# Kernel optimization log

Hardware: AMD Instinct MI355X
Metric: run time of the kernel (lower is better)

## Reference

```python
import jax, jax.numpy as jnp
import numpy as np

HIDDEN = 128
EDGE = 64
EPS = 1e-5

def setup_inputs() -> dict:
    key = jax.random.key(0)
    ks = jax.random.split(key, 12)
    B, N, D = 8, 256, HIDDEN
    h = jax.random.normal(ks[0], (B, N, D), dtype=jnp.float32)
    edge_feats = jax.random.normal(ks[1], (B, N, N, 3), dtype=jnp.float32)
    adj_mask = jax.random.bernoulli(ks[2], 0.5, (B, N, N))
    s = lambda fan_in: 1.0 / np.sqrt(fan_in)
    W1 = jax.random.uniform(ks[3], (D + 3, EDGE), minval=-s(D + 3), maxval=s(D + 3))
    b1 = jnp.zeros((EDGE,), jnp.float32)
    W2 = jax.random.uniform(ks[4], (EDGE, D), minval=-s(EDGE), maxval=s(EDGE))
    b2 = jnp.zeros((D,), jnp.float32)
    U1 = jax.random.uniform(ks[5], (3 * D, D), minval=-s(3 * D), maxval=s(3 * D))
    b3 = jnp.zeros((D,), jnp.float32)
    U2 = jax.random.uniform(ks[6], (D, D), minval=-s(D), maxval=s(D))
    b4 = jnp.zeros((D,), jnp.float32)
    gamma = jnp.ones((D,), jnp.float32)
    beta = jnp.zeros((D,), jnp.float32)
    return {"h": h, "edge_feats": edge_feats, "adj_mask": adj_mask,
            "W1": W1, "b1": b1, "W2": W2, "b2": b2,
            "U1": U1, "b3": b3, "U2": U2, "b4": b4,
            "gamma": gamma, "beta": beta}

def reference(h, edge_feats, adj_mask, W1, b1, W2, b2, U1, b3, U2, b4, gamma, beta):
    B, N, D = h.shape
    # NOTE: torch does h.unsqueeze(2).expand(B,N,N,D): h_j[b,i,j,:] = h[b,i,:]
    h_j = jnp.broadcast_to(h[:, :, None, :], (B, N, N, D))
    gate_in = jnp.concatenate([h_j, edge_feats], axis=-1)          # (B,N,N,D+3)
    gates = jax.nn.sigmoid(jax.nn.relu(gate_in @ W1 + b1) @ W2 + b2)  # (B,N,N,D)
    mask_f = adj_mask.astype(h.dtype)[..., None]                    # (B,N,N,1)
    messages = gates * h_j * mask_f
    neighbor_count = jnp.clip(jnp.sum(mask_f, axis=2), 1.0)         # (B,N,1)
    agg_mean = jnp.sum(messages, axis=2) / neighbor_count           # (B,N,D)
    msgs_max = jnp.where(adj_mask[..., None], messages, -jnp.inf)
    agg_max = jnp.max(msgs_max, axis=2)
    agg_max = jnp.where(jnp.isinf(agg_max), 0.0, agg_max)
    upd_in = jnp.concatenate([h, agg_mean, agg_max], axis=-1)       # (B,N,3D)
    upd = jax.nn.relu(upd_in @ U1 + b3) @ U2 + b4
    x = h + upd
    mu = jnp.mean(x, axis=-1, keepdims=True)
    var = jnp.var(x, axis=-1, keepdims=True)
    return (x - mu) * jax.lax.rsqrt(var + EPS) * gamma + beta
```

## Files before the change

kernel.cpp:

```cpp
#include <hip/hip_runtime.h>
#include <hip/hip_bf16.h>
#include <math.h>

#define NN 256
#define DD 128
#define EE 64
#define TPAD 72
#define APAD 392
#define RPAD 136

typedef __attribute__((ext_vector_type(8))) short short8;
typedef __attribute__((ext_vector_type(4))) float f32x4;

static __device__ __forceinline__ unsigned short f2bf(float f) {
    __hip_bfloat16 b = __float2bfloat16(f);
    return *reinterpret_cast<unsigned short*>(&b);
}

static __device__ __forceinline__ short8 ldb(const float* __restrict__ B, int kbase, int d) {
    unsigned short tmp[8];
    #pragma unroll
    for (int j = 0; j < 8; ++j) tmp[j] = f2bf(B[(kbase + j) * DD + d]);
    return *(const short8*)tmp;
}

__global__ __launch_bounds__(256, 3)
void ecgc_gate(const float* __restrict__ h_g,
               const float* __restrict__ ef_g,
               const int*   __restrict__ mask_g,
               const float* __restrict__ W1_g,
               const float* __restrict__ b1_g,
               const float* __restrict__ W2_g,
               const float* __restrict__ b2_g,
               float*       __restrict__ ws)
{
    const int bi   = blockIdx.x;
    const int t    = threadIdx.x;
    const int lane = t & 63;
    const int w    = t >> 6;
    const int m16  = lane & 15;
    const int quad = lane >> 4;

    __shared__ __align__(16) unsigned short shT[NN * TPAD];
    __shared__ __align__(16) float sh_ef[NN * 4];
    __shared__ float sh_h[DD], sh_base[EE], sh_w1e[3 * EE];
    __shared__ int   sh_jlist[NN], sh_wcnt[4], sh_cnt;

    if (t < DD) sh_h[t] = h_g[bi * DD + t];
    {
        const float* efr = ef_g + (size_t)bi * NN * 3;
        sh_ef[t * 4 + 0] = efr[t * 3 + 0];
        sh_ef[t * 4 + 1] = efr[t * 3 + 1];
        sh_ef[t * 4 + 2] = efr[t * 3 + 2];
        sh_ef[t * 4 + 3] = 0.f;
    }
    const int mk = (mask_g[bi * NN + t] != 0) ? 1 : 0;
    const unsigned long long bal = __ballot(mk);
    if (lane == 0) sh_wcnt[w] = __popcll(bal);
    const int pre = __popcll(bal & ((1ull << lane) - 1ull));
    __syncthreads();

    {
        int wbase = 0;
        for (int ww = 0; ww < w; ++ww) wbase += sh_wcnt[ww];
        if (mk) sh_jlist[wbase + pre] = t;
        if (t == 0) sh_cnt = sh_wcnt[0] + sh_wcnt[1] + sh_wcnt[2] + sh_wcnt[3];
    }

    if (t < EE) {
        float acc = b1_g[t];
        #pragma unroll 4
        for (int d = 0; d < DD; ++d)
            acc = fmaf(sh_h[d], W1_g[d * EE + t], acc);
        sh_base[t] = acc;
    } else {
        const int u = t - EE;
        sh_w1e[u] = W1_g[(DD + (u >> 6)) * EE + (u & 63)];
    }

    const int dstripe = w * 32;
    short8 bfrag[2][2];
    float  nb2[2];
    #pragma unroll
    for (int dt = 0; dt < 2; ++dt) {
        const int d = dstripe + 16 * dt + m16;
        nb2[dt] = b2_g[d];
        #pragma unroll
        for (int kh = 0; kh < 2; ++kh)
            bfrag[dt][kh] = ldb(W2_g, kh * 32 + quad * 8, d);
    }
    __syncthreads();

    const int cnt = sh_cnt;
    const int njt = (cnt + 15) >> 4;

    {
        const int cj = t & 63, eg = w;
        for (int c = 0; c < 4; ++c) {
            const int js = c * 64 + cj;
            float e0 = 0.f, e1 = 0.f, e2 = 0.f;
            const int ok = (js < cnt);
            if (ok) {
                const float4 efv = *(const float4*)&sh_ef[sh_jlist[js] * 4];
                e0 = efv.x; e1 = efv.y; e2 = efv.z;
            }
            unsigned short pk[16];
            #pragma unroll
            for (int v = 0; v < 16; ++v) {
                const int e = eg * 16 + v;
                float tv = 0.f;
                if (ok)
                    tv = fmaxf(fmaf(e0, sh_w1e[e],
                               fmaf(e1, sh_w1e[64 + e],
                               fmaf(e2, sh_w1e[128 + e], sh_base[e]))), 0.f);
                pk[v] = f2bf(tv);
            }
            *(short8*)&shT[js * TPAD + eg * 16]     = *(const short8*)&pk[0];
            *(short8*)&shT[js * TPAD + eg * 16 + 8] = *(const short8*)&pk[8];
        }
    }
    __syncthreads();

    float sumv[2] = {0.f, 0.f};
    float mxv[2]  = {-__builtin_inff(), -__builtin_inff()};
    float mnv[2]  = { __builtin_inff(),  __builtin_inff()};

    for (int jt = 0; jt < njt; ++jt) {
        const short8 a0 = *(const short8*)&shT[(jt * 16 + m16) * TPAD + quad * 8];
        const short8 a1 = *(const short8*)&shT[(jt * 16 + m16) * TPAD + 32 + quad * 8];
        const int jbase = jt * 16 + quad * 4;
        #pragma unroll
        for (int dt = 0; dt < 2; ++dt) {
            f32x4 acc = {0.f, 0.f, 0.f, 0.f};
            acc = __builtin_amdgcn_mfma_f32_16x16x32_bf16(a0, bfrag[dt][0], acc, 0, 0, 0);
            acc = __builtin_amdgcn_mfma_f32_16x16x32_bf16(a1, bfrag[dt][1], acc, 0, 0, 0);
            #pragma unroll
            for (int r = 0; r < 4; ++r) {
                const float g = __fdividef(1.f, 1.f + __expf(-(acc[r] + nb2[dt])));
                if (jbase + r < cnt) {
                    sumv[dt] += g;
                    mxv[dt]  = fmaxf(mxv[dt], g);
                    mnv[dt]  = fminf(mnv[dt], g);
                }
            }
        }
    }

    #pragma unroll
    for (int dt = 0; dt < 2; ++dt) {
        float s = sumv[dt], M = mxv[dt], mn = mnv[dt];
        s += __shfl_xor(s, 16, 64);  s += __shfl_xor(s, 32, 64);
        M  = fmaxf(M,  __shfl_xor(M, 16, 64));  M  = fmaxf(M,  __shfl_xor(M, 32, 64));
        mn = fminf(mn, __shfl_xor(mn, 16, 64)); mn = fminf(mn, __shfl_xor(mn, 32, 64));
        if (quad == 0) {
            const int d  = dstripe + 16 * dt + m16;
            const float hd = sh_h[d];
            float mean = 0.f, amax = 0.f;
            if (cnt > 0) {
                mean = hd * s * __fdividef(1.f, (float)cnt);
                amax = (hd >= 0.f) ? hd * M : hd * mn;
            }
            ws[bi * 256 + d]       = mean;
            ws[bi * 256 + 128 + d] = amax;
        }
    }
}

__global__ __launch_bounds__(256, 2)
void ecgc_upd(const float* __restrict__ h_g,
              const float* __restrict__ ws,
              const float* __restrict__ U1_g,
              const float* __restrict__ b3_g,
              const float* __restrict__ U2_g,
              const float* __restrict__ b4_g,
              const float* __restrict__ gam_g,
              const float* __restrict__ bet_g,
              float*       __restrict__ out_g)
{
    const int bi0  = blockIdx.x * 32;
    const int t    = threadIdx.x;
    const int lane = t & 63;
    const int w    = t >> 6;
    const int m16  = lane & 15;
    const int quad = lane >> 4;

    __shared__ __align__(16) unsigned short shA[32 * APAD];
    __shared__ __align__(16) unsigned short rbuf[32 * RPAD];
    __shared__ float sh_s[4 * 32], sh_s2[4 * 32], sh_mu[32], sh_rs[32];

    {
        const int row = t >> 3, q = t & 7;
        const float* srcs[3] = { h_g + (size_t)(bi0 + row) * DD + q * 16,
                                 ws  + (size_t)(bi0 + row) * 256 + q * 16,
                                 ws  + (size_t)(bi0 + row) * 256 + 128 + q * 16 };
        #pragma unroll
        for (int seg = 0; seg < 3; ++seg) {
            const float4* sp = (const float4*)srcs[seg];
            unsigned short tmp[16];
            #pragma unroll
            for (int vv = 0; vv < 4; ++vv) {
                const float4 v = sp[vv];
                tmp[vv * 4 + 0] = f2bf(v.x); tmp[vv * 4 + 1] = f2bf(v.y);
                tmp[vv * 4 + 2] = f2bf(v.z); tmp[vv * 4 + 3] = f2bf(v.w);
            }
            *(short8*)&shA[row * APAD + seg * DD + q * 16]     = *(const short8*)&tmp[0];
            *(short8*)&shA[row * APAD + seg * DD + q * 16 + 8] = *(const short8*)&tmp[8];
        }
    }
    __syncthreads();

    const int dstripe = w * 32;

    f32x4 acc[2][2];
    #pragma unroll
    for (int mt = 0; mt < 2; ++mt)
        #pragma unroll
        for (int dt = 0; dt < 2; ++dt) acc[mt][dt] = (f32x4){0.f, 0.f, 0.f, 0.f};

    for (int kk = 0; kk < 12; ++kk) {
        const short8 a0 = *(const short8*)&shA[m16 * APAD + kk * 32 + quad * 8];
        const short8 a1 = *(const short8*)&shA[(16 + m16) * APAD + kk * 32 + quad * 8];
        #pragma unroll
        for (int dt = 0; dt < 2; ++dt) {
            const short8 b = ldb(U1_g, kk * 32 + quad * 8, dstripe + dt * 16 + m16);
            acc[0][dt] = __builtin_amdgcn_mfma_f32_16x16x32_bf16(a0, b, acc[0][dt], 0, 0, 0);
            acc[1][dt] = __builtin_amdgcn_mfma_f32_16x16x32_bf16(a1, b, acc[1][dt], 0, 0, 0);
        }
    }

    #pragma unroll
    for (int mt = 0; mt < 2; ++mt)
        #pragma unroll
        for (int dt = 0; dt < 2; ++dt) {
            const int d = dstripe + dt * 16 + m16;
            const float bb = b3_g[d];
            #pragma unroll
            for (int r = 0; r < 4; ++r) {
                const int ro = mt * 16 + quad * 4 + r;
                rbuf[ro * RPAD + d] = f2bf(fmaxf(acc[mt][dt][r] + bb, 0.f));
            }
        }
    __syncthreads();

    f32x4 acc2[2][2];
    #pragma unroll
    for (int mt = 0; mt < 2; ++mt)
        #pragma unroll
        for (int dt = 0; dt < 2; ++dt) acc2[mt][dt] = (f32x4){0.f, 0.f, 0.f, 0.f};

    for (int kk = 0; kk < 4; ++kk) {
        const short8 a0 = *(const short8*)&rbuf[m16 * RPAD + kk * 32 + quad * 8];
        const short8 a1 = *(const short8*)&rbuf[(16 + m16) * RPAD + kk * 32 + quad * 8];
        #pragma unroll
        for (int dt = 0; dt < 2; ++dt) {
            const short8 b = ldb(U2_g, kk * 32 + quad * 8, dstripe + dt * 16 + m16);
            acc2[0][dt] = __builtin_amdgcn_mfma_f32_16x16x32_bf16(a0, b, acc2[0][dt], 0, 0, 0);
            acc2[1][dt] = __builtin_amdgcn_mfma_f32_16x16x32_bf16(a1, b, acc2[1][dt], 0, 0, 0);
        }
    }

    float xv[2][2][4];
    #pragma unroll
    for (int mt = 0; mt < 2; ++mt)
        #pragma unroll
        for (int dt = 0; dt < 2; ++dt) {
            const int d = dstripe + dt * 16 + m16;
            const float bb = b4_g[d];
            #pragma unroll
            for (int r = 0; r < 4; ++r) {
                const int ro = mt * 16 + quad * 4 + r;
                xv[mt][dt][r] = h_g[(size_t)(bi0 + ro) * DD + d] + acc2[mt][dt][r] + bb;
            }
        }

    #pragma unroll
    for (int mt = 0; mt < 2; ++mt)
        #pragma unroll
        for (int r = 0; r < 4; ++r) {
            float s  = xv[mt][0][r] + xv[mt][1][r];
            float s2 = xv[mt][0][r] * xv[mt][0][r] + xv[mt][1][r] * xv[mt][1][r];
            #pragma unroll
            for (int off = 1; off < 16; off <<= 1) {
                s  += __shfl_xor(s,  off, 64);
                s2 += __shfl_xor(s2, off, 64);
            }
            if (m16 == 0) {
                const int ro = mt * 16 + quad * 4 + r;
                sh_s[w * 32 + ro]  = s;
                sh_s2[w * 32 + ro] = s2;
            }
        }
    __syncthreads();
    if (t < 32) {
        const float S  = sh_s[t]  + sh_s[32 + t]  + sh_s[64 + t]  + sh_s[96 + t];
        const float S2 = sh_s2[t] + sh_s2[32 + t] + sh_s2[64 + t] + sh_s2[96 + t];
        const float mu  = S * (1.f / 128.f);
        const float var = S2 * (1.f / 128.f) - mu * mu;
        sh_mu[t] = mu;
        sh_rs[t] = rsqrtf(var + 1e-5f);
    }
    __syncthreads();

    #pragma unroll
    for (int mt = 0; mt < 2; ++mt)
        #pragma unroll
        for (int dt = 0; dt < 2; ++dt) {
            const int d = dstripe + dt * 16 + m16;
            const float ga = gam_g[d], be = bet_g[d];
            #pragma unroll
            for (int r = 0; r < 4; ++r) {
                const int ro = mt * 16 + quad * 4 + r;
                out_g[(size_t)(bi0 + ro) * DD + d] =
                    (xv[mt][dt][r] - sh_mu[ro]) * sh_rs[ro] * ga + be;
            }
        }
}

extern "C" void kernel_launch(void* const* d_in, const int* in_sizes, int n_in,
                              void* d_out, int out_size, void* d_ws, size_t ws_size,
                              hipStream_t stream) {
    float* ws = (float*)d_ws;
    ecgc_gate<<<8 * NN, 256, 0, stream>>>(
        (const float*)d_in[0],
        (const float*)d_in[1],
        (const int*)d_in[2],
        (const float*)d_in[3],
        (const float*)d_in[4],
        (const float*)d_in[5],
        (const float*)d_in[6],
        ws);
    ecgc_upd<<<(8 * NN) / 32, 256, 0, stream>>>(
        (const float*)d_in[0],
        ws,
        (const float*)d_in[7],
        (const float*)d_in[8],
        (const float*)d_in[9],
        (const float*)d_in[10],
        (const float*)d_in[11],
        (const float*)d_in[12],
        (float*)d_out);
}
```

Measured before the change: 140.1 us.

## Chunk gate tile to shrink LDS, parallelize base GEMV, halve upd block rows

Result: faster. 125.5 us (-10.4%).

```diff
diff --git a/kernel.cpp b/kernel.cpp
--- a/kernel.cpp
+++ b/kernel.cpp
@@ -24,7 +24,7 @@
     return *(const short8*)tmp;
 }
 
-__global__ __launch_bounds__(256, 3)
+__global__ __launch_bounds__(256, 6)
 void ecgc_gate(const float* __restrict__ h_g,
                const float* __restrict__ ef_g,
                const int*   __restrict__ mask_g,
@@ -41,12 +41,16 @@
     const int m16  = lane & 15;
     const int quad = lane >> 4;
 
-    __shared__ __align__(16) unsigned short shT[NN * TPAD];
+    __shared__ __align__(16) unsigned short shT[64 * TPAD];
     __shared__ __align__(16) float sh_ef[NN * 4];
-    __shared__ float sh_h[DD], sh_base[EE], sh_w1e[3 * EE];
+    __shared__ __align__(16) float sh_base[EE];
+    __shared__ __align__(16) float sh_w1e[3 * EE];
+    __shared__ float sh_h[DD];
+    __shared__ float sh_basep[4 * EE];
     __shared__ int   sh_jlist[NN], sh_wcnt[4], sh_cnt;
 
     if (t < DD) sh_h[t] = h_g[bi * DD + t];
+    if (t < 192) sh_w1e[t] = W1_g[(DD + (t >> 6)) * EE + (t & 63)];
     {
         const float* efr = ef_g + (size_t)bi * NN * 3;
         sh_ef[t * 4 + 0] = efr[t * 3 + 0];
@@ -58,6 +62,18 @@
     const unsigned long long bal = __ballot(mk);
     if (lane == 0) sh_wcnt[w] = __popcll(bal);
     const int pre = __popcll(bal & ((1ull << lane) - 1ull));
+
+    const int dstripe = w * 32;
+    short8 bfrag[2][2];
+    float  nb2[2];
+    #pragma unroll
+    for (int dt = 0; dt < 2; ++dt) {
+        const int d = dstripe + 16 * dt + m16;
+        nb2[dt] = b2_g[d];
+        #pragma unroll
+        for (int kh = 0; kh < 2; ++kh)
+            bfrag[dt][kh] = ldb(W2_g, kh * 32 + quad * 8, d);
+    }
     __syncthreads();
 
     {
@@ -66,84 +82,86 @@
         if (mk) sh_jlist[wbase + pre] = t;
         if (t == 0) sh_cnt = sh_wcnt[0] + sh_wcnt[1] + sh_wcnt[2] + sh_wcnt[3];
     }
-
-    if (t < EE) {
-        float acc = b1_g[t];
+    {
+        const int e = t & 63, dgrp = t >> 6;
+        float acc = 0.f;
         #pragma unroll 4
-        for (int d = 0; d < DD; ++d)
-            acc = fmaf(sh_h[d], W1_g[d * EE + t], acc);
-        sh_base[t] = acc;
-    } else {
-        const int u = t - EE;
-        sh_w1e[u] = W1_g[(DD + (u >> 6)) * EE + (u & 63)];
-    }
-
-    const int dstripe = w * 32;
-    short8 bfrag[2][2];
-    float  nb2[2];
-    #pragma unroll
-    for (int dt = 0; dt < 2; ++dt) {
-        const int d = dstripe + 16 * dt + m16;
-        nb2[dt] = b2_g[d];
-        #pragma unroll
-        for (int kh = 0; kh < 2; ++kh)
-            bfrag[dt][kh] = ldb(W2_g, kh * 32 + quad * 8, d);
-    }
+        for (int d = dgrp * 32; d < dgrp * 32 + 32; ++d)
+            acc = fmaf(sh_h[d], W1_g[d * EE + e], acc);
+        sh_basep[dgrp * EE + e] = acc;
+    }
+    __syncthreads();
+    if (t < EE)
+        sh_base[t] = b1_g[t] + sh_basep[t] + sh_basep[EE + t] +
+                     sh_basep[2 * EE + t] + sh_basep[3 * EE + t];
     __syncthreads();
 
     const int cnt = sh_cnt;
-    const int njt = (cnt + 15) >> 4;
-
-    {
-        const int cj = t & 63, eg = w;
-        for (int c = 0; c < 4; ++c) {
-            const int js = c * 64 + cj;
-            float e0 = 0.f, e1 = 0.f, e2 = 0.f;
-            const int ok = (js < cnt);
+    const int nch = (cnt + 63) >> 6;
+
+    float sumv[2] = {0.f, 0.f};
+    float mxv[2]  = {-__builtin_inff(), -__builtin_inff()};
+    float mnv[2]  = { __builtin_inff(),  __builtin_inff()};
+
+    for (int ch = 0; ch < nch; ++ch) {
+        {
+            const int row = t >> 2, e0 = (t & 3) * 16;
+            const int js  = ch * 64 + row;
+            const int ok  = (js < cnt);
+            float e0f = 0.f, e1f = 0.f, e2f = 0.f;
             if (ok) {
                 const float4 efv = *(const float4*)&sh_ef[sh_jlist[js] * 4];
-                e0 = efv.x; e1 = efv.y; e2 = efv.z;
+                e0f = efv.x; e1f = efv.y; e2f = efv.z;
             }
             unsigned short pk[16];
             #pragma unroll
-            for (int v = 0; v < 16; ++v) {
-                const int e = eg * 16 + v;
-                float tv = 0.f;
-                if (ok)
-                    tv = fmaxf(fmaf(e0, sh_w1e[e],
-                               fmaf(e1, sh_w1e[64 + e],
-                               fmaf(e2, sh_w1e[128 + e], sh_base[e]))), 0.f);
-                pk[v] = f2bf(tv);
-            }
-            *(short8*)&shT[js * TPAD + eg * 16]     = *(const short8*)&pk[0];
-            *(short8*)&shT[js * TPAD + eg * 16 + 8] = *(const short8*)&pk[8];
-        }
-    }
-    __syncthreads();
-
-    float sumv[2] = {0.f, 0.f};
-    float mxv[2]  = {-__builtin_inff(), -__builtin_inff()};
-    float mnv[2]  = { __builtin_inff(),  __builtin_inff()};
-
-    for (int jt = 0; jt < njt; ++jt) {
-        const short8 a0 = *(const short8*)&shT[(jt * 16 + m16) * TPAD + quad * 8];
-        const short8 a1 = *(const short8*)&shT[(jt * 16 + m16) * TPAD + 32 + quad * 8];
-        const int jbase = jt * 16 + quad * 4;
-        #pragma unroll
-        for (int dt = 0; dt < 2; ++dt) {
-            f32x4 acc = {0.f, 0.f, 0.f, 0.f};
-            acc = __builtin_amdgcn_mfma_f32_16x16x32_bf16(a0, bfrag[dt][0], acc, 0, 0, 0);
-            acc = __builtin_amdgcn_mfma_f32_16x16x32_bf16(a1, bfrag[dt][1], acc, 0, 0, 0);
-            #pragma unroll
-            for (int r = 0; r < 4; ++r) {
-                const float g = __fdividef(1.f, 1.f + __expf(-(acc[r] + nb2[dt])));
-                if (jbase + r < cnt) {
-                    sumv[dt] += g;
-                    mxv[dt]  = fmaxf(mxv[dt], g);
-                    mnv[dt]  = fminf(mnv[dt], g);
+            for (int vb = 0; vb < 4; ++vb) {
+                const float4 bs = *(const float4*)&sh_base[e0 + vb * 4];
+                const float4 w0 = *(const float4*)&sh_w1e[e0 + vb * 4];
+                const float4 w1 = *(const float4*)&sh_w1e[64 + e0 + vb * 4];
+                const float4 w2 = *(const float4*)&sh_w1e[128 + e0 + vb * 4];
+                const float bsx[4] = {bs.x, bs.y, bs.z, bs.w};
+                const float w0x[4] = {w0.x, w0.y, w0.z, w0.w};
+                const float w1x[4] = {w1.x, w1.y, w1.z, w1.w};
+                const float w2x[4] = {w2.x, w2.y, w2.z, w2.w};
+                #pragma unroll
+                for (int v = 0; v < 4; ++v) {
+                    float tv = 0.f;
+                    if (ok)
+                        tv = fmaxf(fmaf(e0f, w0x[v],
+                                   fmaf(e1f, w1x[v],
+                                   fmaf(e2f, w2x[v], bsx[v]))), 0.f);
+                    pk[vb * 4 + v] = f2bf(tv);
                 }
             }
-        }
+            *(short8*)&shT[row * TPAD + e0]     = *(const short8*)&pk[0];
+            *(short8*)&shT[row * TPAD + e0 + 8] = *(const short8*)&pk[8];
+        }
+        __syncthreads();
+
+        const int rem = min(64, cnt - ch * 64);
+        const int jtn = (rem + 15) >> 4;
+        for (int jt = 0; jt < jtn; ++jt) {
+            const short8 a0 = *(const short8*)&shT[(jt * 16 + m16) * TPAD + quad * 8];
+            const short8 a1 = *(const short8*)&shT[(jt * 16 + m16) * TPAD + 32 + quad * 8];
+            const int jbase = ch * 64 + jt * 16 + quad * 4;
+            #pragma unroll
+            for (int dt = 0; dt < 2; ++dt) {
+                f32x4 acc = {0.f, 0.f, 0.f, 0.f};
+                acc = __builtin_amdgcn_mfma_f32_16x16x32_bf16(a0, bfrag[dt][0], acc, 0, 0, 0);
+                acc = __builtin_amdgcn_mfma_f32_16x16x32_bf16(a1, bfrag[dt][1], acc, 0, 0, 0);
+                #pragma unroll
+                for (int r = 0; r < 4; ++r) {
+                    const float g = __fdividef(1.f, 1.f + __expf(-(acc[r] + nb2[dt])));
+                    if (jbase + r < cnt) {
+                        sumv[dt] += g;
+                        mxv[dt]  = fmaxf(mxv[dt], g);
+                        mnv[dt]  = fminf(mnv[dt], g);
+                    }
+                }
+            }
+        }
+        __syncthreads();
     }
 
     #pragma unroll
@@ -177,123 +195,102 @@
               const float* __restrict__ bet_g,
               float*       __restrict__ out_g)
 {
-    const int bi0  = blockIdx.x * 32;
+    const int bi0  = blockIdx.x * 16;
     const int t    = threadIdx.x;
     const int lane = t & 63;
     const int w    = t >> 6;
     const int m16  = lane & 15;
     const int quad = lane >> 4;
 
-    __shared__ __align__(16) unsigned short shA[32 * APAD];
-    __shared__ __align__(16) unsigned short rbuf[32 * RPAD];
-    __shared__ float sh_s[4 * 32], sh_s2[4 * 32], sh_mu[32], sh_rs[32];
+    __shared__ __align__(16) unsigned short shA[16 * APAD];
+    __shared__ __align__(16) unsigned short rbuf[16 * RPAD];
+    __shared__ float sh_s[4 * 16], sh_s2[4 * 16], sh_mu[16], sh_rs[16];
 
     {
-        const int row = t >> 3, q = t & 7;
-        const float* srcs[3] = { h_g + (size_t)(bi0 + row) * DD + q * 16,
-                                 ws  + (size_t)(bi0 + row) * 256 + q * 16,
-                                 ws  + (size_t)(bi0 + row) * 256 + 128 + q * 16 };
-        #pragma unroll
-        for (int seg = 0; seg < 3; ++seg) {
-            const float4* sp = (const float4*)srcs[seg];
-            unsigned short tmp[16];
-            #pragma unroll
-            for (int vv = 0; vv < 4; ++vv) {
-                const float4 v = sp[vv];
-                tmp[vv * 4 + 0] = f2bf(v.x); tmp[vv * 4 + 1] = f2bf(v.y);
-                tmp[vv * 4 + 2] = f2bf(v.z); tmp[vv * 4 + 3] = f2bf(v.w);
-            }
-            *(short8*)&shA[row * APAD + seg * DD + q * 16]     = *(const short8*)&tmp[0];
-            *(short8*)&shA[row * APAD + seg * DD + q * 16 + 8] = *(const short8*)&tmp[8];
-        }
+        const int row = t >> 4, q = t & 15;
+        const float* hrow = h_g + (size_t)(bi0 + row) * DD;
+        const float* wrow = ws  + (size_t)(bi0 + row) * 256;
+        unsigned short tmp[24];
+        #pragma unroll
+        for (int c = 0; c < 24; ++c) {
+            const int col = q * 24 + c;
+            float v;
+            if (col < 128)      v = hrow[col];
+            else if (col < 256) v = wrow[col - 128];
+            else                v = wrow[col - 256 + 128];
+            tmp[c] = f2bf(v);
+        }
+        #pragma unroll
+        for (int s8 = 0; s8 < 3; ++s8)
+            *(short8*)&shA[row * APAD + q * 24 + s8 * 8] = *(const short8*)&tmp[s8 * 8];
     }
     __syncthreads();
 
     const int dstripe = w * 32;
 
-    f32x4 acc[2][2];
-    #pragma unroll
-    for (int mt = 0; mt < 2; ++mt)
-        #pragma unroll
-        for (int dt = 0; dt < 2; ++dt) acc[mt][dt] = (f32x4){0.f, 0.f, 0.f, 0.f};
-
+    f32x4 acc[2] = {{0.f, 0.f, 0.f, 0.f}, {0.f, 0.f, 0.f, 0.f}};
     for (int kk = 0; kk < 12; ++kk) {
         const short8 a0 = *(const short8*)&shA[m16 * APAD + kk * 32 + quad * 8];
-        const short8 a1 = *(const short8*)&shA[(16 + m16) * APAD + kk * 32 + quad * 8];
         #pragma unroll
         for (int dt = 0; dt < 2; ++dt) {
             const short8 b = ldb(U1_g, kk * 32 + quad * 8, dstripe + dt * 16 + m16);
-            acc[0][dt] = __builtin_amdgcn_mfma_f32_16x16x32_bf16(a0, b, acc[0][dt], 0, 0, 0);
-            acc[1][dt] = __builtin_amdgcn_mfma_f32_16x16x32_bf16(a1, b, acc[1][dt], 0, 0, 0);
-        }
-    }
-
-    #pragma unroll
-    for (int mt = 0; mt < 2; ++mt)
-        #pragma unroll
-        for (int dt = 0; dt < 2; ++dt) {
-            const int d = dstripe + dt * 16 + m16;
-            const float bb = b3_g[d];
-            #pragma unroll
-            for (int r = 0; r < 4; ++r) {
-                const int ro = mt * 16 + quad * 4 + r;
-                rbuf[ro * RPAD + d] = f2bf(fmaxf(acc[mt][dt][r] + bb, 0.f));
-            }
-        }
-    __syncthreads();
-
-    f32x4 acc2[2][2];
-    #pragma unroll
-    for (int mt = 0; mt < 2; ++mt)
-        #pragma unroll
-        for (int dt = 0; dt < 2; ++dt) acc2[mt][dt] = (f32x4){0.f, 0.f, 0.f, 0.f};
-
+            acc[dt] = __builtin_amdgcn_mfma_f32_16x16x32_bf16(a0, b, acc[dt], 0, 0, 0);
+        }
+    }
+
+    #pragma unroll
+    for (int dt = 0; dt < 2; ++dt) {
+        const int d = dstripe + dt * 16 + m16;
+        const float bb = b3_g[d];
+        #pragma unroll
+        for (int r = 0; r < 4; ++r) {
+            const int ro = quad * 4 + r;
+            rbuf[ro * RPAD + d] = f2bf(fmaxf(acc[dt][r] + bb, 0.f));
+        }
+    }
+    __syncthreads();
+
+    f32x4 acc2[2] = {{0.f, 0.f, 0.f, 0.f}, {0.f, 0.f, 0.f, 0.f}};
     for (int kk = 0; kk < 4; ++kk) {
         const short8 a0 = *(const short8*)&rbuf[m16 * RPAD + kk * 32 + quad * 8];
-        const short8 a1 = *(const short8*)&rbuf[(16 + m16) * RPAD + kk * 32 + quad * 8];
         #pragma unroll
         for (int dt = 0; dt < 2; ++dt) {
             const short8 b = ldb(U2_g, kk * 32 + quad * 8, dstripe + dt * 16 + m16);
-            acc2[0][dt] = __builtin_amdgcn_mfma_f32_16x16x32_bf16(a0, b, acc2[0][dt], 0, 0, 0);
-            acc2[1][dt] = __builtin_amdgcn_mfma_f32_16x16x32_bf16(a1, b, acc2[1][dt], 0, 0, 0);
-        }
-    }
-
-    float xv[2][2][4];
-    #pragma unroll
-    for (int mt = 0; mt < 2; ++mt)
-        #pragma unroll
-        for (int dt = 0; dt < 2; ++dt) {
-            const int d = dstripe + dt * 16 + m16;
-            const float bb = b4_g[d];
-            #pragma unroll
-            for (int r = 0; r < 4; ++r) {
-                const int ro = mt * 16 + quad * 4 + r;
-                xv[mt][dt][r] = h_g[(size_t)(bi0 + ro) * DD + d] + acc2[mt][dt][r] + bb;
-            }
-        }
-
-    #pragma unroll
-    for (int mt = 0; mt < 2; ++mt)
+            acc2[dt] = __builtin_amdgcn_mfma_f32_16x16x32_bf16(a0, b, acc2[dt], 0, 0, 0);
+        }
+    }
+
+    float xv[2][4];
+    #pragma unroll
+    for (int dt = 0; dt < 2; ++dt) {
+        const int d = dstripe + dt * 16 + m16;
+        const float bb = b4_g[d];
         #pragma unroll
         for (int r = 0; r < 4; ++r) {
-            float s  = xv[mt][0][r] + xv[mt][1][r];
-            float s2 = xv[mt][0][r] * xv[mt][0][r] + xv[mt][1][r] * xv[mt][1][r];
-            #pragma unroll
-            for (int off = 1; off < 16; off <<= 1) {
-                s  += __shfl_xor(s,  off, 64);
-                s2 += __shfl_xor(s2, off, 64);
-            }
-            if (m16 == 0) {
-                const int ro = mt * 16 + quad * 4 + r;
-                sh_s[w * 32 + ro]  = s;
-                sh_s2[w * 32 + ro] = s2;
-            }
-        }
-    __syncthreads();
-    if (t < 32) {
-        const float S  = sh_s[t]  + sh_s[32 + t]  + sh_s[64 + t]  + sh_s[96 + t];
-        const float S2 = sh_s2[t] + sh_s2[32 + t] + sh_s2[64 + t] + sh_s2[96 + t];
+            const int ro = quad * 4 + r;
+            xv[dt][r] = h_g[(size_t)(bi0 + ro) * DD + d] + acc2[dt][r] + bb;
+        }
+    }
+
+    #pragma unroll
+    for (int r = 0; r < 4; ++r) {
+        float s  = xv[0][r] + xv[1][r];
+        float s2 = xv[0][r] * xv[0][r] + xv[1][r] * xv[1][r];
+        #pragma unroll
+        for (int off = 1; off < 16; off <<= 1) {
+            s  += __shfl_xor(s,  off, 64);
+            s2 += __shfl_xor(s2, off, 64);
+        }
+        if (m16 == 0) {
+            const int ro = quad * 4 + r;
+            sh_s[w * 16 + ro]  = s;
+            sh_s2[w * 16 + ro] = s2;
+        }
+    }
+    __syncthreads();
+    if (t < 16) {
+        const float S  = sh_s[t]  + sh_s[16 + t]  + sh_s[32 + t]  + sh_s[48 + t];
+        const float S2 = sh_s2[t] + sh_s2[16 + t] + sh_s2[32 + t] + sh_s2[48 + t];
         const float mu  = S * (1.f / 128.f);
         const float var = S2 * (1.f / 128.f) - mu * mu;
         sh_mu[t] = mu;
@@ -302,18 +299,16 @@
     __syncthreads();
 
     #pragma unroll
-    for (int mt = 0; mt < 2; ++mt)
-        #pragma unroll
-        for (int dt = 0; dt < 2; ++dt) {
-            const int d = dstripe + dt * 16 + m16;
-            const float ga = gam_g[d], be = bet_g[d];
-            #pragma unroll
-            for (int r = 0; r < 4; ++r) {
-                const int ro = mt * 16 + quad * 4 + r;
-                out_g[(size_t)(bi0 + ro) * DD + d] =
-                    (xv[mt][dt][r] - sh_mu[ro]) * sh_rs[ro] * ga + be;
-            }
-        }
+    for (int dt = 0; dt < 2; ++dt) {
+        const int d = dstripe + dt * 16 + m16;
+        const float ga = gam_g[d], be = bet_g[d];
+        #pragma unroll
+        for (int r = 0; r < 4; ++r) {
+            const int ro = quad * 4 + r;
+            out_g[(size_t)(bi0 + ro) * DD + d] =
+                (xv[dt][r] - sh_mu[ro]) * sh_rs[ro] * ga + be;
+        }
+    }
 }
 
 extern "C" void kernel_launch(void* const* d_in, const int* in_sizes, int n_in,
@@ -329,7 +324,7 @@
         (const float*)d_in[5],
         (const float*)d_in[6],
         ws);
-    ecgc_upd<<<(8 * NN) / 32, 256, 0, stream>>>(
+    ecgc_upd<<<(8 * NN) / 16, 256, 0, stream>>>(
         (const float*)d_in[0],
         ws,
         (const float*)d_in[7],
```
